# Kernel tuning notes

Measured on AMD Instinct MI355X. Metric: run time of the kernel, lower is better.

Reference implementation:

```python
import jax, jax.numpy as jnp
import numpy as np

B, DIM, HW = 16, 256, 64      # input feature map
G, DH = 8, 64                 # offset_groups = heads = 8, dim_head = 64
DPG = DIM // G                # 32 channels per group
TP = 8                        # tile size: 8x8 grid of 8x8 tiles
DS = 4                        # downsample factor -> 2x2 offset grid per tile
CPB_DIM = DIM // 4            # 64, CPB mlp width
SCALE = DH ** -0.5


def _grid_sample(img, grid):
    # F.grid_sample, bilinear, zero padding, align_corners=False
    # img (N,C,H,W), grid (N,Ho,Wo,2) with last dim (x,y) in [-1,1]
    N, C, H, W = img.shape
    Ho, Wo = grid.shape[1:3]
    x = ((grid[..., 0] + 1.0) * W - 1.0) / 2.0
    y = ((grid[..., 1] + 1.0) * H - 1.0) / 2.0
    x0 = jnp.floor(x)
    y0 = jnp.floor(y)
    imgf = img.reshape(N, C, H * W)
    out = jnp.zeros((N, C, Ho * Wo), img.dtype)
    for dx, wx in ((0.0, x0 + 1.0 - x), (1.0, x - x0)):
        for dy, wy in ((0.0, y0 + 1.0 - y), (1.0, y - y0)):
            ix = x0 + dx
            iy = y0 + dy
            valid = (ix >= 0) & (ix < W) & (iy >= 0) & (iy < H)
            idx = (jnp.clip(iy, 0, H - 1) * W + jnp.clip(ix, 0, W - 1)).astype(jnp.int32)
            idxf = idx.reshape(N, Ho * Wo)
            g = jax.vmap(lambda im, ii: im[:, ii])(imgf, idxf)  # (N,C,HoWo)
            w = (wx * wy * valid).reshape(N, 1, Ho * Wo)
            out = out + g * w
    return out.reshape(N, C, Ho, Wo)


def _forward(x, ln_g, ln_b, wq, wk, wv, off_w1, off_b1, off_w2,
             cpb_w1, cpb_b1, cpb_w2, cpb_b2, cpb_w3, cpb_b3, wo, bo):
    Bb, C, H, W = x.shape
    # LayerNorm over channel dim (eps=1e-6)
    xt = jnp.moveaxis(x, 1, -1)
    mu = xt.mean(-1, keepdims=True)
    var = ((xt - mu) ** 2).mean(-1, keepdims=True)
    xt = (xt - mu) * jax.lax.rsqrt(var + 1e-6) * ln_g + ln_b
    x = jnp.moveaxis(xt, -1, 1)
    # patchify: (b c (i p) (j q)) -> ((i j b) c p q)  [vectorizes the 64-iter python loop]
    xp = x.reshape(Bb, C, 8, TP, 8, TP).transpose(2, 4, 0, 1, 3, 5).reshape(64 * Bb, C, TP, TP)
    N = 64 * Bb
    # grouped 1x1 to_q (groups = offset_groups)
    xg = xp.reshape(N, G, DPG, TP, TP)
    q = jnp.einsum('ngchw,goc->ngohw', xg, wq)          # (N,8,64,8,8)
    gq = q.reshape(N * G, DH, TP, TP)
    # offset net: depthwise conv k=6 s=4 p=1 -> GELU -> 1x1 -> tanh -> *offset_scale
    off = jax.lax.conv_general_dilated(gq, off_w1, (DS, DS), ((1, 1), (1, 1)),
                                       feature_group_count=DH)
    off = jax.nn.gelu(off + off_b1[None, :, None, None], approximate=False)
    off = jnp.tanh(jnp.einsum('nchw,oc->nohw', off, off_w2)) * float(DS)  # (N*G,2,2,2)
    # virtual sampling grid on the 2x2 offset grid, normalized by (size-1)
    r = jnp.arange(2, dtype=x.dtype)
    gx, gy = jnp.meshgrid(r, r, indexing='xy')
    vgrid = jnp.stack([gx, gy])[None] + off              # (N*G,2,2,2) ch=(x,y)
    vnorm = 2.0 * vgrid - 1.0                            # max(2-1,1)=1
    vgrid_s = jnp.moveaxis(vnorm, 1, -1)                 # (N*G,2,2,2) last=(x,y)
    kv = _grid_sample(xp.reshape(N * G, DPG, TP, TP), vgrid_s)   # (N*G,32,2,2)
    kvf = kv.reshape(N, G, DPG, 2, 2)
    k = jnp.einsum('ngchw,goc->ngohw', kvf, wk)          # (N,8,64,2,2)
    v = jnp.einsum('ngchw,goc->ngohw', kvf, wv)
    qh = q.transpose(0, 1, 3, 4, 2).reshape(N, G, TP * TP, DH) * SCALE
    kh = k.transpose(0, 1, 3, 4, 2).reshape(N, G, 4, DH)
    vh = v.transpose(0, 1, 3, 4, 2).reshape(N, G, 4, DH)
    sim = jnp.einsum('bhid,bhjd->bhij', qh, kh)          # (N,8,64,4)
    # continuous position bias (CPB)
    rq = jnp.arange(TP, dtype=x.dtype)
    qx, qy = jnp.meshgrid(rq, rq, indexing='xy')
    gridq = jnp.stack([qx, qy], -1).reshape(TP * TP, 2) * (2.0 / (TP - 1)) - 1.0
    pos = gridq[None, :, None, :] - vgrid_s.reshape(N * G, 1, 4, 2)  # (N*G,64,4,2)
    bz = jnp.sign(pos) * jnp.log1p(jnp.abs(pos))
    bz = jax.nn.relu(bz @ cpb_w1 + cpb_b1)
    bz = jax.nn.relu(bz @ cpb_w2 + cpb_b2)
    bz = (bz @ cpb_w3 + cpb_b3).reshape(N, G, TP * TP, 4)
    attn = jax.nn.softmax(sim + bz, axis=-1)
    out = jnp.einsum('bhij,bhjd->bhid', attn, vh)        # (N,8,64,64)
    out = out.transpose(0, 1, 3, 2).reshape(N, G * DH, TP, TP)
    out = jnp.einsum('nchw,oc->nohw', out, wo) + bo[None, :, None, None]
    # reassemble: ((i j b) c p q) -> (b c (i p) (j q))
    y = out.reshape(8, 8, Bb, C, TP, TP).transpose(2, 3, 0, 4, 1, 5).reshape(Bb, C, H, W)
    return y


def setup_inputs() -> dict:
    key = jax.random.key(0)
    ks = jax.random.split(key, 12)
    s = 0.05
    return {
        'x': jax.random.normal(ks[0], (B, DIM, HW, HW), jnp.float32),
        'ln_g': jnp.ones((DIM,), jnp.float32),
        'ln_b': jnp.zeros((DIM,), jnp.float32),
        'wq': jax.random.normal(ks[1], (G, DH, DPG), jnp.float32) * s,
        'wk': jax.random.normal(ks[2], (G, DH, DPG), jnp.float32) * s,
        'wv': jax.random.normal(ks[3], (G, DH, DPG), jnp.float32) * s,
        'off_w1': jax.random.normal(ks[4], (DH, 1, 6, 6), jnp.float32) * s,
        'off_b1': jnp.zeros((DH,), jnp.float32),
        'off_w2': jax.random.normal(ks[5], (2, DH), jnp.float32) * s,
        'cpb_w1': jax.random.normal(ks[6], (2, CPB_DIM), jnp.float32) * s,
        'cpb_b1': jnp.zeros((CPB_DIM,), jnp.float32),
        'cpb_w2': jax.random.normal(ks[7], (CPB_DIM, CPB_DIM), jnp.float32) * s,
        'cpb_b2': jnp.zeros((CPB_DIM,), jnp.float32),
        'cpb_w3': jax.random.normal(ks[8], (CPB_DIM, 1), jnp.float32) * s,
        'cpb_b3': jnp.zeros((1,), jnp.float32),
        'wo': jax.random.normal(ks[9], (DIM, G * DH), jnp.float32) * s,
        'bo': jnp.zeros((DIM,), jnp.float32),
    }


def reference(x, ln_g, ln_b, wq, wk, wv, off_w1, off_b1, off_w2,
              cpb_w1, cpb_b1, cpb_w2, cpb_b2, cpb_w3, cpb_b3, wo, bo):
    return _forward(x, ln_g, ln_b, wq, wk, wv, off_w1, off_b1, off_w2,
                    cpb_w1, cpb_b1, cpb_w2, cpb_b2, cpb_w3, cpb_b3, wo, bo)
```

## Files before the change

### kernel.cpp

```cpp
#include <hip/hip_runtime.h>
#include <math.h>


#define WS_VN  16777216
#define WS_WOT 16842752

typedef __attribute__((ext_vector_type(8))) short short8;
typedef __attribute__((ext_vector_type(4))) float f32x4;

__device__ __forceinline__ short f2bf(float f) {
  unsigned u = __builtin_bit_cast(unsigned, f);
  u += 0x7fff + ((u >> 16) & 1);
  return (short)(u >> 16);
}
__device__ __forceinline__ float bf2f(short h) {
  return __builtin_bit_cast(float, ((unsigned)(unsigned short)h) << 16);
}

__global__ __launch_bounds__(256) void k1_ln(const float* __restrict__ x,
    const float* __restrict__ ln_g, const float* __restrict__ ln_b,
    float* __restrict__ xn) {
  int blk = blockIdx.x;
  int b = blk >> 6, h = blk & 63;
  int t = threadIdx.x;
  int quarter = t >> 6, wcol = t & 63;
  const float* xrow = x + (size_t)b * (256 * 4096) + h * 64 + wcol;
  float s = 0.f, ss = 0.f;
#pragma unroll 8
  for (int i = 0; i < 64; ++i) {
    float v = xrow[(size_t)(quarter * 64 + i) * 4096];
    s += v; ss += v * v;
  }
  __shared__ float sm[4][64], sq[4][64], mu_s[64], rs_s[64];
  sm[quarter][wcol] = s; sq[quarter][wcol] = ss;
  __syncthreads();
  if (t < 64) {
    float S  = sm[0][t] + sm[1][t] + sm[2][t] + sm[3][t];
    float SS = sq[0][t] + sq[1][t] + sq[2][t] + sq[3][t];
    float mu = S * (1.f / 256.f);
    float var = SS * (1.f / 256.f) - mu * mu;
    mu_s[t] = mu;
    rs_s[t] = 1.f / sqrtf(var + 1e-6f);
  }
  __syncthreads();
  float mu = mu_s[wcol], rs = rs_s[wcol];
  int it = h >> 3, p = h & 7, jt = wcol >> 3, qq = wcol & 7;
  int n = (it * 8 + jt) * 16 + b;
  float* xo = xn + (size_t)n * 16384 + p * 8 + qq;
#pragma unroll 8
  for (int i = 0; i < 64; ++i) {
    int c = quarter * 64 + i;
    float v = xrow[(size_t)c * 4096];
    xo[c * 64] = (v - mu) * rs * ln_g[c] + ln_b[c];
  }
}

__global__ __launch_bounds__(64) void k2_qoff(const float* __restrict__ xn,
    const float* __restrict__ wq, const float* __restrict__ w1,
    const float* __restrict__ b1, const float* __restrict__ w2,
    short* __restrict__ qb, float* __restrict__ vn) {
  int ng = blockIdx.x;
  int n = ng >> 3, g = ng & 7;
  int lane = threadIdx.x;
  __shared__ float qs[64][65];
  __shared__ float os[64][4];
  const float* xb = xn + (size_t)n * 16384 + g * 2048;
  float xr[32];
#pragma unroll
  for (int c = 0; c < 32; ++c) xr[c] = xb[c * 64 + lane];
  const float* wqg = wq + g * 2048;
#pragma unroll 4
  for (int o = 0; o < 64; ++o) {
    float acc = 0.f;
#pragma unroll
    for (int c = 0; c < 32; ++c) acc += wqg[o * 32 + c] * xr[c];
    qs[o][lane] = acc;
  }
  __syncthreads();
  const float* w1c = w1 + lane * 36;
#pragma unroll
  for (int oy = 0; oy < 2; ++oy)
#pragma unroll
    for (int ox = 0; ox < 2; ++ox) {
      float a = 0.f;
#pragma unroll
      for (int ky = 0; ky < 6; ++ky) {
        int iy = oy * 4 - 1 + ky;
        if (iy < 0 || iy > 7) continue;
#pragma unroll
        for (int kx = 0; kx < 6; ++kx) {
          int ix = ox * 4 - 1 + kx;
          if (ix < 0 || ix > 7) continue;
          a += w1c[ky * 6 + kx] * qs[lane][iy * 8 + ix];
        }
      }
      a += b1[lane];
      a = 0.5f * a * (1.f + erff(a * 0.70710678118654752f));
      os[lane][oy * 2 + ox] = a;
    }
  __syncthreads();
  {
    short* qrow = qb + ((size_t)(n * 64 + lane) * 512 + g * 64);
#pragma unroll
    for (int o8 = 0; o8 < 8; ++o8) {
      short8 v8;
#pragma unroll
      for (int j = 0; j < 8; ++j) v8[j] = f2bf(qs[o8 * 8 + j][lane]);
      *(short8*)&qrow[o8 * 8] = v8;
    }
  }
  if (lane < 8) {
    int oc = lane >> 2, s = lane & 3;
    float a = 0.f;
    for (int o = 0; o < 64; ++o) a += w2[oc * 64 + o] * os[o][s];
    float off = tanhf(a) * 4.f;
    float base = (oc == 0) ? (float)(s & 1) : (float)(s >> 1);
    vn[(size_t)ng * 8 + s * 2 + oc] = 2.f * (base + off) - 1.f;
  }
}

__global__ __launch_bounds__(256, 3) void k3_attn(const float* __restrict__ xn,
    const float* __restrict__ wk, const float* __restrict__ wv,
    const float* __restrict__ vn,
    const float* __restrict__ cw1, const float* __restrict__ cb1,
    const float* __restrict__ cw2, const float* __restrict__ cb2,
    const float* __restrict__ cw3, const float* __restrict__ cb3,
    short* __restrict__ qattB) {
  int w = threadIdx.x >> 6;
  int lane = threadIdx.x & 63;
  int ng = blockIdx.x * 4 + w;
  int n = ng >> 3, g = ng & 7;
  __shared__ alignas(16) float kvs[4][32][4];
  __shared__ alignas(16) float ks[4][64][4];
  __shared__ alignas(16) float vs[4][64][4];
  __shared__ alignas(16) short bfragLDS[512 * 8];
  __shared__ float biasS[4][4][64];

  {
    int t = threadIdx.x;
#pragma unroll
    for (int rep = 0; rep < 2; ++rep) {
      int slot = t + rep * 256;
      int combo = slot >> 6, ln = slot & 63;
      int kstep = combo >> 2, nt = combo & 3;
      int kbase = kstep * 32 + (ln >> 4) * 8;
      int ncol = nt * 16 + (ln & 15);
      short8 v;
#pragma unroll
      for (int jj = 0; jj < 8; ++jj) v[jj] = f2bf(cw2[(kbase + jj) * 64 + ncol]);
      *(short8*)&bfragLDS[slot * 8] = v;
    }
  }

  const float* vp = vn + (size_t)ng * 8;
  float vx0 = vp[0], vy0 = vp[1], vx1 = vp[2], vy1 = vp[3];
  float vx2 = vp[4], vy2 = vp[5], vx3 = vp[6], vy3 = vp[7];
  {
    int c = lane & 31, s2 = lane >> 5;
    const float* tile = xn + (size_t)n * 16384 + (g * 32 + c) * 64;
#pragma unroll
    for (int rep = 0; rep < 2; ++rep) {
      int s = s2 + 2 * rep;
      float vxs = (rep == 0) ? (s2 ? vx1 : vx0) : (s2 ? vx3 : vx2);
      float vys = (rep == 0) ? (s2 ? vy1 : vy0) : (s2 ? vy3 : vy2);
      float X = 4.f * vxs + 3.5f, Y = 4.f * vys + 3.5f;
      float x0f = floorf(X), y0f = floorf(Y);
      int x0 = (int)x0f, y0 = (int)y0f;
      float wx1 = X - x0f, wy1 = Y - y0f;
      float acc = 0.f;
      for (int dy = 0; dy < 2; ++dy) {
        int iy = y0 + dy;
        if (iy < 0 || iy > 7) continue;
        float wyv = dy ? wy1 : 1.f - wy1;
        for (int dx = 0; dx < 2; ++dx) {
          int ix = x0 + dx;
          if (ix < 0 || ix > 7) continue;
          float wxv = dx ? wx1 : 1.f - wx1;
          acc += tile[iy * 8 + ix] * wxv * wyv;
        }
      }
      kvs[w][c][s] = acc;
    }
  }
  __syncthreads();
  {
    int d = lane;
    float ka0 = 0, ka1 = 0, ka2 = 0, ka3 = 0, va0 = 0, va1 = 0, va2 = 0, va3 = 0;
    const float4* wk4 = (const float4*)(wk + g * 2048 + d * 32);
    const float4* wv4 = (const float4*)(wv + g * 2048 + d * 32);
#pragma unroll
    for (int c4 = 0; c4 < 8; ++c4) {
      float4 a4 = wk4[c4], b4 = wv4[c4];
      float aw[4] = {a4.x, a4.y, a4.z, a4.w};
      float bw[4] = {b4.x, b4.y, b4.z, b4.w};
#pragma unroll
      for (int u = 0; u < 4; ++u) {
        float4 kv4 = *(const float4*)kvs[w][c4 * 4 + u];
        ka0 += aw[u] * kv4.x; ka1 += aw[u] * kv4.y;
        ka2 += aw[u] * kv4.z; ka3 += aw[u] * kv4.w;
        va0 += bw[u] * kv4.x; va1 += bw[u] * kv4.y;
        va2 += bw[u] * kv4.z; va3 += bw[u] * kv4.w;
      }
    }
    ks[w][d][0] = ka0; ks[w][d][1] = ka1; ks[w][d][2] = ka2; ks[w][d][3] = ka3;
    vs[w][d][0] = va0; vs[w][d][1] = va1; vs[w][d][2] = va2; vs[w][d][3] = va3;
  }
  __syncthreads();
  float sim0 = 0, sim1 = 0, sim2 = 0, sim3 = 0;
  short* qrow = qattB + ((size_t)(n * 64 + lane) * 512 + g * 64);
#pragma unroll 2
  for (int d8 = 0; d8 < 8; ++d8) {
    short8 q8 = *(const short8*)&qrow[d8 * 8];
#pragma unroll
    for (int j = 0; j < 8; ++j) {
      float qv = bf2f(q8[j]);
      float4 k4 = *(const float4*)ks[w][d8 * 8 + j];
      sim0 += qv * k4.x; sim1 += qv * k4.y; sim2 += qv * k4.z; sim3 += qv * k4.w;
    }
  }
  float logit0 = sim0 * 0.125f, logit1 = sim1 * 0.125f;
  float logit2 = sim2 * 0.125f, logit3 = sim3 * 0.125f;

  short8 bf[2][4];
#pragma unroll
  for (int kstep = 0; kstep < 2; ++kstep)
#pragma unroll
    for (int nt = 0; nt < 4; ++nt)
      bf[kstep][nt] = *(const short8*)&bfragLDS[((kstep * 4 + nt) * 64 + lane) * 8];
  int kcol = (lane >> 4) * 8;
  float c1x[16], c1y[16], c1b[16];
#pragma unroll
  for (int ks2 = 0; ks2 < 2; ++ks2)
#pragma unroll
    for (int jj = 0; jj < 8; ++jj) {
      int i = ks2 * 32 + kcol + jj;
      c1x[ks2 * 8 + jj] = cw1[i];
      c1y[ks2 * 8 + jj] = cw1[64 + i];
      c1b[ks2 * 8 + jj] = cb1[i];
    }
  int jme = lane & 15;
  float w3v[4], b2v[4];
#pragma unroll
  for (int nt = 0; nt < 4; ++nt) {
    w3v[nt] = cw3[nt * 16 + jme];
    b2v[nt] = cb2[nt * 16 + jme];
  }
  float gqx = (float)(jme & 7) * (2.f / 7.f) - 1.f;
  float yrow = (float)(jme >> 3);
#pragma unroll 1
  for (int s = 0; s < 4; ++s) {
    float vxs = (s == 0) ? vx0 : (s == 1) ? vx1 : (s == 2) ? vx2 : vx3;
    float vys = (s == 0) ? vy0 : (s == 1) ? vy1 : (s == 2) ? vy2 : vy3;
    float px = gqx - vxs;
    float tx = copysignf(log1pf(fabsf(px)), px);
    float pre[16];
#pragma unroll
    for (int t2 = 0; t2 < 16; ++t2) pre[t2] = fmaf(tx, c1x[t2], c1b[t2]);
#pragma unroll 1
    for (int mt4 = 0; mt4 < 4; ++mt4) {
      float gqy = (float)(mt4 * 2) * (2.f / 7.f) + yrow * (2.f / 7.f) - 1.f;
      float py = gqy - vys;
      float ty = copysignf(log1pf(fabsf(py)), py);
      short8 af[2];
#pragma unroll
      for (int ks2 = 0; ks2 < 2; ++ks2)
#pragma unroll
        for (int jj = 0; jj < 8; ++jj) {
          float h = fmaxf(fmaf(ty, c1y[ks2 * 8 + jj], pre[ks2 * 8 + jj]), 0.f);
          af[ks2][jj] = f2bf(h);
        }
      f32x4 a0 = {0,0,0,0}, a1 = {0,0,0,0}, a2 = {0,0,0,0}, a3 = {0,0,0,0};
      a0 = __builtin_amdgcn_mfma_f32_16x16x32_bf16(af[0], bf[0][0], a0, 0, 0, 0);
      a0 = __builtin_amdgcn_mfma_f32_16x16x32_bf16(af[1], bf[1][0], a0, 0, 0, 0);
      a1 = __builtin_amdgcn_mfma_f32_16x16x32_bf16(af[0], bf[0][1], a1, 0, 0, 0);
      a1 = __builtin_amdgcn_mfma_f32_16x16x32_bf16(af[1], bf[1][1], a1, 0, 0, 0);
      a2 = __builtin_amdgcn_mfma_f32_16x16x32_bf16(af[0], bf[0][2], a2, 0, 0, 0);
      a2 = __builtin_amdgcn_mfma_f32_16x16x32_bf16(af[1], bf[1][2], a2, 0, 0, 0);
      a3 = __builtin_amdgcn_mfma_f32_16x16x32_bf16(af[0], bf[0][3], a3, 0, 0, 0);
      a3 = __builtin_amdgcn_mfma_f32_16x16x32_bf16(af[1], bf[1][3], a3, 0, 0, 0);
      float part[4];
#pragma unroll
      for (int reg = 0; reg < 4; ++reg) {
        part[reg] = w3v[0] * fmaxf(a0[reg] + b2v[0], 0.f)
                  + w3v[1] * fmaxf(a1[reg] + b2v[1], 0.f)
                  + w3v[2] * fmaxf(a2[reg] + b2v[2], 0.f)
                  + w3v[3] * fmaxf(a3[reg] + b2v[3], 0.f);
      }
#pragma unroll
      for (int st = 1; st < 16; st <<= 1)
#pragma unroll
        for (int reg = 0; reg < 4; ++reg)
          part[reg] += __shfl_xor(part[reg], st, 64);
      if (jme == 0) {
        int posO = mt4 * 16 + (lane >> 4) * 4;
#pragma unroll
        for (int reg = 0; reg < 4; ++reg) biasS[w][s][posO + reg] = part[reg];
      }
    }
  }
  __syncthreads();
  float c3 = cb3[0];
  logit0 += biasS[w][0][lane] + c3;
  logit1 += biasS[w][1][lane] + c3;
  logit2 += biasS[w][2][lane] + c3;
  logit3 += biasS[w][3][lane] + c3;
  float m = fmaxf(fmaxf(logit0, logit1), fmaxf(logit2, logit3));
  float e0 = expf(logit0 - m), e1 = expf(logit1 - m);
  float e2 = expf(logit2 - m), e3 = expf(logit3 - m);
  float inv = 1.f / (e0 + e1 + e2 + e3);
  e0 *= inv; e1 *= inv; e2 *= inv; e3 *= inv;
#pragma unroll 2
  for (int d8 = 0; d8 < 8; ++d8) {
    short8 o8;
#pragma unroll
    for (int j = 0; j < 8; ++j) {
      float4 v4 = *(const float4*)vs[w][d8 * 8 + j];
      o8[j] = f2bf(e0 * v4.x + e1 * v4.y + e2 * v4.z + e3 * v4.w);
    }
    *(short8*)&qrow[d8 * 8] = o8;
  }
}

__global__ __launch_bounds__(256) void k4_cvt(const float* __restrict__ wo,
    short* __restrict__ woH, short* __restrict__ woL) {
  int idx = blockIdx.x * 256 + threadIdx.x;
  float v = wo[idx];
  short hi = f2bf(v);
  woH[idx] = hi;
  woL[idx] = f2bf(v - bf2f(hi));
}

__global__ __launch_bounds__(256) void k4_mfma(const short* __restrict__ attB,
    const short* __restrict__ woH, const short* __restrict__ woL,
    const float* __restrict__ bo, float* __restrict__ y) {
  int n = blockIdx.x;
  int w = threadIdx.x >> 6;
  int lane = threadIdx.x & 63;
  f32x4 acc[4][4];
#pragma unroll
  for (int mt = 0; mt < 4; ++mt)
#pragma unroll
    for (int nt = 0; nt < 4; ++nt) acc[mt][nt] = (f32x4){0.f, 0.f, 0.f, 0.f};
  const short* ab = attB + (size_t)n * 32768;
  int ncol0 = w * 64 + (lane & 15);
  int mr = lane & 15, kq = (lane >> 4) * 8;
#pragma unroll 2
  for (int kst = 0; kst < 16; ++kst) {
    int k0 = kst * 32 + kq;
    short8 a[4];
#pragma unroll
    for (int mt = 0; mt < 4; ++mt)
      a[mt] = *(const short8*)&ab[(mt * 16 + mr) * 512 + k0];
#pragma unroll
    for (int nt = 0; nt < 4; ++nt) {
      size_t off = (size_t)(ncol0 + nt * 16) * 512 + k0;
      short8 bhi = *(const short8*)&woH[off];
      short8 blo = *(const short8*)&woL[off];
#pragma unroll
      for (int mt = 0; mt < 4; ++mt) {
        acc[mt][nt] = __builtin_amdgcn_mfma_f32_16x16x32_bf16(a[mt], bhi, acc[mt][nt], 0, 0, 0);
        acc[mt][nt] = __builtin_amdgcn_mfma_f32_16x16x32_bf16(a[mt], blo, acc[mt][nt], 0, 0, 0);
      }
    }
  }
  int b = n & 15, jt = (n >> 4) & 7, it = n >> 7;
#pragma unroll
  for (int nt = 0; nt < 4; ++nt) {
    int o = w * 64 + nt * 16 + (lane & 15);
    float bov = bo[o];
    size_t ybase = ((size_t)b * 256 + o) * 4096;
#pragma unroll
    for (int mt = 0; mt < 4; ++mt) {
#pragma unroll
      for (int reg = 0; reg < 4; ++reg) {
        int row = mt * 16 + (lane >> 4) * 4 + reg;
        int h = it * 8 + (row >> 3), wc = jt * 8 + (row & 7);
        y[ybase + h * 64 + wc] = acc[mt][nt][reg] + bov;
      }
    }
  }
}

extern "C" void kernel_launch(void* const* d_in, const int* in_sizes, int n_in,
                              void* d_out, int out_size, void* d_ws, size_t ws_size,
                              hipStream_t stream) {
  (void)in_sizes; (void)n_in; (void)out_size; (void)ws_size;
  const float* x    = (const float*)d_in[0];
  const float* ln_g = (const float*)d_in[1];
  const float* ln_b = (const float*)d_in[2];
  const float* wq   = (const float*)d_in[3];
  const float* wk   = (const float*)d_in[4];
  const float* wv   = (const float*)d_in[5];
  const float* ow1  = (const float*)d_in[6];
  const float* ob1  = (const float*)d_in[7];
  const float* ow2  = (const float*)d_in[8];
  const float* cw1  = (const float*)d_in[9];
  const float* cb1  = (const float*)d_in[10];
  const float* cw2  = (const float*)d_in[11];
  const float* cb2  = (const float*)d_in[12];
  const float* cw3  = (const float*)d_in[13];
  const float* cb3  = (const float*)d_in[14];
  const float* wo   = (const float*)d_in[15];
  const float* bo   = (const float*)d_in[16];
  float* y  = (float*)d_out;
  float* ws = (float*)d_ws;
  short* qattB = (short*)ws;
  float* vnb   = ws + WS_VN;
  short* woH   = (short*)(ws + WS_WOT);
  short* woL   = woH + 131072;
  float* xn = y;

  k4_cvt<<<512, 256, 0, stream>>>(wo, woH, woL);
  k1_ln<<<1024, 256, 0, stream>>>(x, ln_g, ln_b, xn);
  k2_qoff<<<8192, 64, 0, stream>>>(xn, wq, ow1, ob1, ow2, qattB, vnb);
  k3_attn<<<2048, 256, 0, stream>>>(xn, wk, wv, vnb, cw1, cb1, cw2, cb2,
                                    cw3, cb3, qattB);
  k4_mfma<<<1024, 256, 0, stream>>>(qattB, woH, woL, bo, y);
}
```

Measured before the change: 493.1 us.

## Compute grouped q projection with split-bf16 MFMA and parallelize offset net

Replaces the scalar FP32 grouped 1x1 q projection in k2_qoff with bf16 MFMA 16x16x32, using a hi/lo split of weights and activations (three MFMAs) to keep near-FP32 accuracy. A new small kernel pre-converts wq into hi/lo bf16 arrays. Blocks now hold four waves, each handling one output offset position, and loop over four groups. The offset 1x1 conv becomes a wave-wide shuffle reduction instead of an 8-lane serial loop. This cuts scalar FMA work and serial tail latency, at the cost of an extra launch and a small precision change from dropping the lo*lo term.

```diff
diff --git a/kernel.cpp b/kernel.cpp
--- a/kernel.cpp
+++ b/kernel.cpp
@@ -6,6 +6,7 @@
 #define WS_WOT 16842752
 
 typedef __attribute__((ext_vector_type(8))) short short8;
+typedef __attribute__((ext_vector_type(4))) short short4b;
 typedef __attribute__((ext_vector_type(4))) float f32x4;
 
 __device__ __forceinline__ short f2bf(float f) {
@@ -55,67 +56,95 @@
   }
 }
 
-__global__ __launch_bounds__(64) void k2_qoff(const float* __restrict__ xn,
-    const float* __restrict__ wq, const float* __restrict__ w1,
-    const float* __restrict__ b1, const float* __restrict__ w2,
-    short* __restrict__ qb, float* __restrict__ vn) {
-  int ng = blockIdx.x;
-  int n = ng >> 3, g = ng & 7;
-  int lane = threadIdx.x;
+__global__ __launch_bounds__(256) void k0_cvtwq(const float* __restrict__ wq,
+    short* __restrict__ wqH, short* __restrict__ wqL) {
+  int idx = blockIdx.x * 256 + threadIdx.x;
+  float v = wq[idx];
+  short hi = f2bf(v);
+  wqH[idx] = hi;
+  wqL[idx] = f2bf(v - bf2f(hi));
+}
+
+__global__ __launch_bounds__(256, 4) void k2_qoff(const float* __restrict__ xn,
+    const short* __restrict__ wqH, const short* __restrict__ wqL,
+    const float* __restrict__ w1, const float* __restrict__ b1,
+    const float* __restrict__ w2, short* __restrict__ qb,
+    float* __restrict__ vn) {
+  int blk = blockIdx.x;
+  int n = blk >> 1, gh = blk & 1;
+  int w = threadIdx.x >> 6;
+  int lane = threadIdx.x & 63;
+  int l15 = lane & 15, q4 = lane >> 4;
   __shared__ float qs[64][65];
-  __shared__ float os[64][4];
-  const float* xb = xn + (size_t)n * 16384 + g * 2048;
-  float xr[32];
-#pragma unroll
-  for (int c = 0; c < 32; ++c) xr[c] = xb[c * 64 + lane];
-  const float* wqg = wq + g * 2048;
-#pragma unroll 4
-  for (int o = 0; o < 64; ++o) {
-    float acc = 0.f;
-#pragma unroll
-    for (int c = 0; c < 32; ++c) acc += wqg[o * 32 + c] * xr[c];
-    qs[o][lane] = acc;
-  }
-  __syncthreads();
+
   const float* w1c = w1 + lane * 36;
-#pragma unroll
-  for (int oy = 0; oy < 2; ++oy)
-#pragma unroll
-    for (int ox = 0; ox < 2; ++ox) {
-      float a = 0.f;
-#pragma unroll
-      for (int ky = 0; ky < 6; ++ky) {
-        int iy = oy * 4 - 1 + ky;
-        if (iy < 0 || iy > 7) continue;
-#pragma unroll
-        for (int kx = 0; kx < 6; ++kx) {
-          int ix = ox * 4 - 1 + kx;
-          if (ix < 0 || ix > 7) continue;
-          a += w1c[ky * 6 + kx] * qs[lane][iy * 8 + ix];
-        }
-      }
-      a += b1[lane];
-      a = 0.5f * a * (1.f + erff(a * 0.70710678118654752f));
-      os[lane][oy * 2 + ox] = a;
-    }
-  __syncthreads();
-  {
-    short* qrow = qb + ((size_t)(n * 64 + lane) * 512 + g * 64);
-#pragma unroll
-    for (int o8 = 0; o8 < 8; ++o8) {
-      short8 v8;
-#pragma unroll
-      for (int j = 0; j < 8; ++j) v8[j] = f2bf(qs[o8 * 8 + j][lane]);
-      *(short8*)&qrow[o8 * 8] = v8;
-    }
-  }
-  if (lane < 8) {
-    int oc = lane >> 2, s = lane & 3;
+  float b1v = b1[lane];
+  float w2a = w2[lane];
+  float w2b = w2[64 + lane];
+  int oy = w >> 1, ox = w & 1;
+  int posc = w * 16 + l15;
+
+  for (int gi = 0; gi < 4; ++gi) {
+    int g = gh * 4 + gi;
+    int ng = n * 8 + g;
+    const float* xb = xn + (size_t)n * 16384 + g * 2048;
+    short8 BH, BL;
+#pragma unroll
+    for (int j = 0; j < 8; ++j) {
+      float v = xb[(q4 * 8 + j) * 64 + posc];
+      short hi = f2bf(v);
+      BH[j] = hi;
+      BL[j] = f2bf(v - bf2f(hi));
+    }
+    const short* wqHg = wqH + g * 2048;
+    const short* wqLg = wqL + g * 2048;
+    short* qrow = qb + ((size_t)(n * 64 + posc) * 512 + g * 64);
+#pragma unroll
+    for (int mt = 0; mt < 4; ++mt) {
+      short8 AH = *(const short8*)&wqHg[(mt * 16 + l15) * 32 + q4 * 8];
+      short8 AL = *(const short8*)&wqLg[(mt * 16 + l15) * 32 + q4 * 8];
+      f32x4 acc = {0.f, 0.f, 0.f, 0.f};
+      acc = __builtin_amdgcn_mfma_f32_16x16x32_bf16(AH, BH, acc, 0, 0, 0);
+      acc = __builtin_amdgcn_mfma_f32_16x16x32_bf16(AL, BH, acc, 0, 0, 0);
+      acc = __builtin_amdgcn_mfma_f32_16x16x32_bf16(AH, BL, acc, 0, 0, 0);
+      int obase = mt * 16 + q4 * 4;
+#pragma unroll
+      for (int reg = 0; reg < 4; ++reg) qs[obase + reg][posc] = acc[reg];
+      short4b qv;
+#pragma unroll
+      for (int reg = 0; reg < 4; ++reg) qv[reg] = f2bf(acc[reg]);
+      *(short4b*)&qrow[obase] = qv;
+    }
+    __syncthreads();
     float a = 0.f;
-    for (int o = 0; o < 64; ++o) a += w2[oc * 64 + o] * os[o][s];
-    float off = tanhf(a) * 4.f;
-    float base = (oc == 0) ? (float)(s & 1) : (float)(s >> 1);
-    vn[(size_t)ng * 8 + s * 2 + oc] = 2.f * (base + off) - 1.f;
+#pragma unroll
+    for (int ky = 0; ky < 6; ++ky) {
+      int iy = oy * 4 - 1 + ky;
+      if (iy < 0 || iy > 7) continue;
+#pragma unroll
+      for (int kx = 0; kx < 6; ++kx) {
+        int ix = ox * 4 - 1 + kx;
+        if (ix < 0 || ix > 7) continue;
+        a += w1c[ky * 6 + kx] * qs[lane][iy * 8 + ix];
+      }
+    }
+    a += b1v;
+    a = 0.5f * a * (1.f + erff(a * 0.70710678118654752f));
+    float p0 = w2a * a, p1 = w2b * a;
+#pragma unroll
+    for (int st = 1; st < 64; st <<= 1) {
+      p0 += __shfl_xor(p0, st, 64);
+      p1 += __shfl_xor(p1, st, 64);
+    }
+    if (lane == 0) {
+      float offx = tanhf(p0) * 4.f;
+      float offy = tanhf(p1) * 4.f;
+      float2 o2;
+      o2.x = 2.f * ((float)ox + offx) - 1.f;
+      o2.y = 2.f * ((float)oy + offy) - 1.f;
+      *(float2*)&vn[(size_t)ng * 8 + w * 2] = o2;
+    }
+    __syncthreads();
   }
 }
 
@@ -408,11 +437,14 @@
   float* vnb   = ws + WS_VN;
   short* woH   = (short*)(ws + WS_WOT);
   short* woL   = woH + 131072;
+  short* wqH   = woL + 131072;
+  short* wqL   = wqH + 16384;
   float* xn = y;
 
   k4_cvt<<<512, 256, 0, stream>>>(wo, woH, woL);
+  k0_cvtwq<<<64, 256, 0, stream>>>(wq, wqH, wqL);
   k1_ln<<<1024, 256, 0, stream>>>(x, ln_g, ln_b, xn);
-  k2_qoff<<<8192, 64, 0, stream>>>(xn, wq, ow1, ob1, ow2, qattB, vnb);
+  k2_qoff<<<2048, 256, 0, stream>>>(xn, wqH, wqL, ow1, ob1, ow2, qattB, vnb);
   k3_attn<<<2048, 256, 0, stream>>>(xn, wk, wv, vnb, cw1, cb1, cw2, cb2,
                                     cw3, cb3, qattB);
   k4_mfma<<<1024, 256, 0, stream>>>(qattB, woH, woL, bo, y);
```

Measured after the change: 421.7 us. 1.17x faster.
